# Performance work log

Measured on AMD Instinct MI355X. Metric: run time of the kernel, lower is better.

Reference implementation:

```python
import jax, jax.numpy as jnp
import numpy as np

T = 8192
C = 768
HEAD = 64

def setup_inputs() -> dict:
    key = jax.random.key(0)
    k0, k1, k2, k3 = jax.random.split(key, 4)
    tokens = jax.random.normal(k0, (T, C), dtype=jnp.float32)
    Wk = jax.random.normal(k1, (C, HEAD), dtype=jnp.float32) * (1.0 / np.sqrt(C))
    Wq = jax.random.normal(k2, (C, HEAD), dtype=jnp.float32) * (1.0 / np.sqrt(C))
    Wv = jax.random.normal(k3, (C, HEAD), dtype=jnp.float32) * (1.0 / np.sqrt(C))
    return {"tokens": tokens, "Wk": Wk, "Wq": Wq, "Wv": Wv}

def reference(tokens, Wk, Wq, Wv):
    # Single-head causal attention, faithful to source (scale = C**0.5, a multiply).
    keys = tokens @ Wk          # [T, H]
    queries = tokens @ Wq       # [T, H]
    values = tokens @ Wv        # [T, H]
    c = tokens.shape[-1]
    wei = (queries @ keys.T) * (c ** 0.5)                 # [T, T]
    causal = jnp.tril(jnp.ones((tokens.shape[0], tokens.shape[0]), dtype=bool))
    wei = jnp.where(causal, wei, -jnp.inf)
    wei = jax.nn.softmax(wei, axis=-1)
    return wei @ values         # [T, H]; dropout inactive (training=False)
```

## Files before the change

### kernel.cpp

```cpp
#include <hip/hip_runtime.h>
#include <math.h>

#define T_TOK 8192
#define C_DIM 768
#define H_DIM 64
#define SCALE_LOG2E (27.712812921102035f * 1.4426950408889634f)
#define NSPLIT 4

typedef _Float16 half8 __attribute__((ext_vector_type(8)));
typedef float floatx4 __attribute__((ext_vector_type(4)));

#define MFMA16(a, b, c) __builtin_amdgcn_mfma_f32_16x16x32_f16(a, b, c, 0, 0, 0)
#define WAIT_LGKM0() __builtin_amdgcn_s_waitcnt(0xC07F)
#define EXP2F(x) __builtin_amdgcn_exp2f(x)

typedef __attribute__((address_space(3))) void lds_void;
typedef const __attribute__((address_space(1))) void gbl_void;
#define GLOAD16(gp, lp) \
    __builtin_amdgcn_global_load_lds((gbl_void*)(gp), (lds_void*)(lp), 16, 0, 0)

template <int K> struct IC { static constexpr int v = K; };


__global__ __launch_bounds__(64) void wconvert_kernel(
    const float* __restrict__ Wk, const float* __restrict__ Wq,
    const float* __restrict__ Wv, _Float16* __restrict__ WF)
{
    const int b = blockIdx.x;
    const int mat = b / 96, rem = b % 96, kt = rem >> 2, nb = rem & 3;
    const int lane = threadIdx.x & 63, l15 = lane & 15, quad = lane >> 4;
    const float* __restrict__ W = (mat == 0) ? Wk : (mat == 1) ? Wq : Wv;

    half8 h, l;
#pragma unroll
    for (int j = 0; j < 8; ++j) {
        const float v = W[(kt * 32 + quad * 8 + j) * H_DIM + nb * 16 + l15];
        const _Float16 hv = (_Float16)v;
        h[j] = hv;
        l[j] = (_Float16)(v - (float)hv);
    }
    _Float16* dst = WF + ((((size_t)mat * 24 + kt) * 4 + nb) * 2) * 512 + lane * 8;
    *(half8*)dst = h;
    *(half8*)(dst + 512) = l;
}

__global__ __launch_bounds__(64, 1) void proj_kernel(
    const float* __restrict__ tokens, const _Float16* __restrict__ WF,
    _Float16* __restrict__ KF, _Float16* __restrict__ QF,
    _Float16* __restrict__ VF)
{
    __shared__ __align__(16) char smemraw[40960];
    const int b = blockIdx.x;
    const int lane = threadIdx.x & 63, l15 = lane & 15, quad = lane >> 4;
    const int row0 = b * 32;

    floatx4 acc[3][2][4];
#pragma unroll
    for (int mat = 0; mat < 3; ++mat)
#pragma unroll
        for (int mb = 0; mb < 2; ++mb)
#pragma unroll
            for (int nb = 0; nb < 4; ++nb) acc[mat][mb][nb] = 0;

    const float* __restrict__ xb0 = tokens + (size_t)(row0 + l15) * C_DIM + quad * 8;
    const float* __restrict__ xb1 = tokens + (size_t)(row0 + 16 + l15) * C_DIM + quad * 8;


    {
        _Float16* wb0 = (_Float16*)smemraw;
#pragma unroll
        for (int nb = 0; nb < 4; ++nb) {
            const _Float16* gK = WF + (size_t)((0 * 4 + nb) * 2) * 512 + lane * 8;
            const _Float16* gQ =
                WF + (size_t)(((1 * 24) * 4 + nb) * 2) * 512 + lane * 8;
            const _Float16* gV =
                WF + (size_t)(((2 * 24) * 4 + nb) * 2) * 512 + lane * 8;
            GLOAD16(gK,       wb0 + (nb * 2 + 0) * 512);
            GLOAD16(gK + 512, wb0 + (nb * 2 + 1) * 512);
            GLOAD16(gQ,       wb0 + (8 + nb * 2 + 0) * 512);
            GLOAD16(gQ + 512, wb0 + (8 + nb * 2 + 1) * 512);
            GLOAD16(gV,       wb0 + (16 + nb) * 512);
        }
    }
    __builtin_amdgcn_sched_barrier(0);
    float4 tf[4][4];
#pragma unroll
    for (int d = 0; d < 4; ++d) {
        tf[d][0] = *(const float4*)(xb0 + d * 32);
        tf[d][1] = *(const float4*)(xb0 + d * 32 + 4);
        tf[d][2] = *(const float4*)(xb1 + d * 32);
        tf[d][3] = *(const float4*)(xb1 + d * 32 + 4);
    }
    __builtin_amdgcn_sched_barrier(0);

    auto iter = [&](auto kc) {
        constexpr int kt = decltype(kc)::v;
        constexpr int slot = kt & 3;
        constexpr int curb = kt & 1;
        _Float16* wb  = (_Float16*)(smemraw + curb * 20480);
        _Float16* wbn = (_Float16*)(smemraw + (curb ^ 1) * 20480);

        __builtin_amdgcn_sched_barrier(0);
        const float4 x0 = tf[slot][0], x1 = tf[slot][1];
        const float4 x2 = tf[slot][2], x3 = tf[slot][3];
        __builtin_amdgcn_sched_barrier(0);

        if constexpr (kt < 23) {
            constexpr int ktn = kt + 1;
#pragma unroll
            for (int nb = 0; nb < 4; ++nb) {
                const _Float16* gK =
                    WF + (size_t)((ktn * 4 + nb) * 2) * 512 + lane * 8;
                const _Float16* gQ =
                    WF + (size_t)(((24 + ktn) * 4 + nb) * 2) * 512 + lane * 8;
                const _Float16* gV =
                    WF + (size_t)(((48 + ktn) * 4 + nb) * 2) * 512 + lane * 8;
                GLOAD16(gK,       wbn + (nb * 2 + 0) * 512);
                GLOAD16(gK + 512, wbn + (nb * 2 + 1) * 512);
                GLOAD16(gQ,       wbn + (8 + nb * 2 + 0) * 512);
                GLOAD16(gQ + 512, wbn + (8 + nb * 2 + 1) * 512);
                GLOAD16(gV,       wbn + (16 + nb) * 512);
            }
        }
        __builtin_amdgcn_sched_barrier(0);
        if constexpr (kt + 4 < 24) {
            constexpr int ktf = kt + 4;
            tf[slot][0] = *(const float4*)(xb0 + ktf * 32);
            tf[slot][1] = *(const float4*)(xb0 + ktf * 32 + 4);
            tf[slot][2] = *(const float4*)(xb1 + ktf * 32);
            tf[slot][3] = *(const float4*)(xb1 + ktf * 32 + 4);
        }
        __builtin_amdgcn_sched_barrier(0);
        constexpr int VMN = (kt == 0)
            ? 40
            : ((kt <= 20 ? 4 : 0) + (kt <= 22 ? 20 : 0) + (kt <= 19 ? 4 : 0));
        asm volatile("s_waitcnt vmcnt(%0)" ::"n"(VMN));
        __builtin_amdgcn_sched_barrier(0);

        half8 ah[2], al[2];
        {
            const float xs0[8] = {x0.x, x0.y, x0.z, x0.w, x1.x, x1.y, x1.z, x1.w};
            const float xs1[8] = {x2.x, x2.y, x2.z, x2.w, x3.x, x3.y, x3.z, x3.w};
#pragma unroll
            for (int e = 0; e < 8; ++e) {
                _Float16 hv = (_Float16)xs0[e];
                ah[0][e] = hv;
                al[0][e] = (_Float16)(xs0[e] - (float)hv);
                hv = (_Float16)xs1[e];
                ah[1][e] = hv;
                al[1][e] = (_Float16)(xs1[e] - (float)hv);
            }
        }
        const _Float16* wp = wb + lane * 8;
#pragma unroll
        for (int nb = 0; nb < 4; ++nb) {
            const half8 kh = *(const half8*)(wp + (nb * 2 + 0) * 512);
            const half8 kl = *(const half8*)(wp + (nb * 2 + 1) * 512);
            const half8 qh = *(const half8*)(wp + (8 + nb * 2 + 0) * 512);
            const half8 ql = *(const half8*)(wp + (8 + nb * 2 + 1) * 512);
            const half8 vh = *(const half8*)(wp + (16 + nb) * 512);
#pragma unroll
            for (int mb = 0; mb < 2; ++mb) {
                acc[0][mb][nb] = MFMA16(ah[mb], kh, acc[0][mb][nb]);
                acc[0][mb][nb] = MFMA16(ah[mb], kl, acc[0][mb][nb]);
                acc[0][mb][nb] = MFMA16(al[mb], kh, acc[0][mb][nb]);
                acc[1][mb][nb] = MFMA16(ah[mb], qh, acc[1][mb][nb]);
                acc[1][mb][nb] = MFMA16(ah[mb], ql, acc[1][mb][nb]);
                acc[1][mb][nb] = MFMA16(al[mb], qh, acc[1][mb][nb]);
                acc[2][mb][nb] = MFMA16(ah[mb], vh, acc[2][mb][nb]);
            }
        }
    };
#define PITER(k) iter(IC<k>{});
    PITER(0)  PITER(1)  PITER(2)  PITER(3)  PITER(4)  PITER(5)
    PITER(6)  PITER(7)  PITER(8)  PITER(9)  PITER(10) PITER(11)
    PITER(12) PITER(13) PITER(14) PITER(15) PITER(16) PITER(17)
    PITER(18) PITER(19) PITER(20) PITER(21) PITER(22) PITER(23)
#undef PITER

    __builtin_amdgcn_wave_barrier();
    WAIT_LGKM0();
    __builtin_amdgcn_wave_barrier();

    float* Cb = (float*)smemraw;
#pragma unroll
    for (int mat = 0; mat < 3; ++mat)
#pragma unroll
        for (int mb = 0; mb < 2; ++mb)
#pragma unroll
            for (int nb = 0; nb < 4; ++nb)
#pragma unroll
                for (int r = 0; r < 4; ++r)
                    Cb[mat * 2176 + (mb * 16 + quad * 4 + r) * 68 + nb * 16 + l15] =
                        acc[mat][mb][nb][r];
    __builtin_amdgcn_wave_barrier();
    WAIT_LGKM0();
    __builtin_amdgcn_wave_barrier();

#pragma unroll
    for (int nbL = 0; nbL < 2; ++nbL) {
#pragma unroll
        for (int ks = 0; ks < 2; ++ks) {
            {
                const float* cp = Cb + (nbL * 16 + l15) * 68 + ks * 32 + quad * 8;
                const float4 c0 = *(const float4*)cp;
                const float4 c1 = *(const float4*)(cp + 4);
                const float cs[8] = {c0.x, c0.y, c0.z, c0.w, c1.x, c1.y, c1.z, c1.w};
                half8 h, l;
#pragma unroll
                for (int e = 0; e < 8; ++e) {
                    const _Float16 hv = (_Float16)cs[e];
                    h[e] = hv;
                    l[e] = (_Float16)(cs[e] - (float)hv);
                }
                const int t = b >> 1, nb = (b & 1) * 2 + nbL;
                _Float16* dst =
                    KF + (((size_t)(t * 4 + nb) * 2 + ks) * 2) * 512 + lane * 8;
                *(half8*)dst = h;
                *(half8*)(dst + 512) = l;
            }
            {
                const float* cp =
                    Cb + 2176 + (nbL * 16 + l15) * 68 + ks * 32 + quad * 8;
                const float4 c0 = *(const float4*)cp;
                const float4 c1 = *(const float4*)(cp + 4);
                const float cs[8] = {c0.x, c0.y, c0.z, c0.w, c1.x, c1.y, c1.z, c1.w};
                half8 h, l;
#pragma unroll
                for (int e = 0; e < 8; ++e) {
                    const _Float16 hv = (_Float16)cs[e];
                    h[e] = hv;
                    l[e] = (_Float16)(cs[e] - (float)hv);
                }
                const int rb = b * 2 + nbL;
                _Float16* dst = QF + (((size_t)rb * 2 + ks) * 2) * 512 + lane * 8;
                *(half8*)dst = h;
                *(half8*)(dst + 512) = l;
            }
        }
    }

    {
        const int t = b >> 1, ks = b & 1;
#pragma unroll
        for (int nb = 0; nb < 4; ++nb) {
            half8 h;
#pragma unroll
            for (int j = 0; j < 8; ++j)
                h[j] = (_Float16)Cb[2 * 2176 + (quad * 8 + j) * 68 + nb * 16 + l15];
            *(half8*)(VF + ((size_t)(t * 4 + nb) * 2 + ks) * 512 + lane * 8) = h;
        }
    }
}

__global__ __launch_bounds__(512, 2) void attn_mfma_kernel(
    const _Float16* __restrict__ QF, const _Float16* __restrict__ KF,
    const _Float16* __restrict__ VF,
    float* __restrict__ pm, float* __restrict__ pl, float* __restrict__ po)
{
    __shared__ __align__(16) float smemf[9216];
    _Float16* Ps = (_Float16*)smemf;

    const int w = threadIdx.x >> 6, lane = threadIdx.x & 63;
    const int l15 = lane & 15, quad = lane >> 4;
    const int mhalf = w & 1, ss = w >> 1;

    const int b = blockIdx.x;
    const int j = b & 255, hb = b >> 8;
    const int qt = (hb == 0) ? (j >> 1) : (127 - (j >> 1));
    const int sp = (hb << 1) | (j & 1);

    const int qbase = qt * 64;
    const int wrow0 = qbase + mhalf * 32;

    half8 qh[2][2], ql[2][2];
#pragma unroll
    for (int mb = 0; mb < 2; ++mb)
#pragma unroll
        for (int ks = 0; ks < 2; ++ks) {
            const int rb = qt * 4 + mhalf * 2 + mb;
            const _Float16* qp = QF + (((size_t)rb * 2 + ks) * 2) * 512 + lane * 8;
            qh[mb][ks] = *(const half8*)qp;
            ql[mb][ks] = *(const half8*)(qp + 512);
        }

    floatx4 O[2][4];
#pragma unroll
    for (int mb = 0; mb < 2; ++mb)
#pragma unroll
        for (int nb = 0; nb < 4; ++nb) O[mb][nb] = 0;
    float mreg[2][4], lreg[2][4];
#pragma unroll
    for (int mb = 0; mb < 2; ++mb)
#pragma unroll
        for (int r = 0; r < 4; ++r) { mreg[mb][r] = -INFINITY; lreg[mb][r] = 0.f; }

    const int t0 = sp + 4 * ss;
    half8 bh[4][2], bl[4][2];
    if (t0 <= qt) {
#pragma unroll
        for (int nb = 0; nb < 4; ++nb)
#pragma unroll
            for (int ks = 0; ks < 2; ++ks) {
                const _Float16* kp =
                    KF + (((size_t)(t0 * 4 + nb) * 2 + ks) * 2) * 512 + lane * 8;
                bh[nb][ks] = *(const half8*)kp;
                bl[nb][ks] = *(const half8*)(kp + 512);
            }
    }

    for (int t = t0; t <= qt; t += 16) {
        const int kb = t * 64;

        half8 v0r[4], v1r[4];
#pragma unroll
        for (int nb = 0; nb < 4; ++nb) {
            const _Float16* vp = VF + ((size_t)(t * 4 + nb) * 2) * 512 + lane * 8;
            v0r[nb] = *(const half8*)vp;
            v1r[nb] = *(const half8*)(vp + 512);
        }

        float sv[2][4][4];
#pragma unroll
        for (int mb = 0; mb < 2; ++mb)
#pragma unroll
            for (int nb = 0; nb < 4; ++nb) {
                floatx4 s = 0;
#pragma unroll
                for (int ks = 0; ks < 2; ++ks) {
                    s = MFMA16(qh[mb][ks], bh[nb][ks], s);
                    s = MFMA16(qh[mb][ks], bl[nb][ks], s);
                    s = MFMA16(ql[mb][ks], bh[nb][ks], s);
                }
#pragma unroll
                for (int r = 0; r < 4; ++r) sv[mb][nb][r] = s[r] * SCALE_LOG2E;
            }

        if (t + 16 <= qt) {
            const int tn = t + 16;
#pragma unroll
            for (int nb = 0; nb < 4; ++nb)
#pragma unroll
                for (int ks = 0; ks < 2; ++ks) {
                    const _Float16* kp =
                        KF + (((size_t)(tn * 4 + nb) * 2 + ks) * 2) * 512 + lane * 8;
                    bh[nb][ks] = *(const half8*)kp;
                    bl[nb][ks] = *(const half8*)(kp + 512);
                }
        }

        if (kb + 63 > wrow0) {
#pragma unroll
            for (int mb = 0; mb < 2; ++mb) {
                const int rowbase = wrow0 + mb * 16 + quad * 4;
#pragma unroll
                for (int nb = 0; nb < 4; ++nb) {
                    const int col = kb + nb * 16 + l15;
#pragma unroll
                    for (int r = 0; r < 4; ++r)
                        if (col > rowbase + r) sv[mb][nb][r] = -INFINITY;
                }
            }
        }

#pragma unroll
        for (int mb = 0; mb < 2; ++mb) {
#pragma unroll
            for (int r = 0; r < 4; ++r) {
                float rm = fmaxf(fmaxf(sv[mb][0][r], sv[mb][1][r]),
                                 fmaxf(sv[mb][2][r], sv[mb][3][r]));
                rm = fmaxf(rm, __shfl_xor(rm, 1));
                rm = fmaxf(rm, __shfl_xor(rm, 2));
                rm = fmaxf(rm, __shfl_xor(rm, 4));
                rm = fmaxf(rm, __shfl_xor(rm, 8));
                const float mnew = fmaxf(mreg[mb][r], rm);
                const float alpha = EXP2F(mreg[mb][r] - mnew);
                float psum = 0.f;
#pragma unroll
                for (int nb = 0; nb < 4; ++nb) {
                    const float p = EXP2F(sv[mb][nb][r] - mnew);
                    psum += p;
                    Ps[(w * 2 + mb) * 1152 + (quad * 4 + r) * 72 + nb * 16 + l15] =
                        (_Float16)p;
                }
                lreg[mb][r] = lreg[mb][r] * alpha + psum;
                mreg[mb][r] = mnew;
#pragma unroll
                for (int nb = 0; nb < 4; ++nb) O[mb][nb][r] *= alpha;
            }
        }

        __builtin_amdgcn_wave_barrier();
        WAIT_LGKM0();
        __builtin_amdgcn_wave_barrier();
        half8 pa0[2], pa1[2];
#pragma unroll
        for (int mb = 0; mb < 2; ++mb) {
            const _Float16* pp = Ps + (w * 2 + mb) * 1152 + l15 * 72 + quad * 8;
            pa0[mb] = *(const half8*)pp;
            pa1[mb] = *(const half8*)(pp + 32);
        }

#pragma unroll
        for (int nb = 0; nb < 4; ++nb) {
#pragma unroll
            for (int mb = 0; mb < 2; ++mb) {
                O[mb][nb] = MFMA16(pa0[mb], v0r[nb], O[mb][nb]);
                O[mb][nb] = MFMA16(pa1[mb], v1r[nb], O[mb][nb]);
            }
        }
        __builtin_amdgcn_wave_barrier();
    }

#pragma unroll
    for (int mb = 0; mb < 2; ++mb)
#pragma unroll
        for (int r = 0; r < 4; ++r) {
            float s = lreg[mb][r];
            s += __shfl_xor(s, 1);
            s += __shfl_xor(s, 2);
            s += __shfl_xor(s, 4);
            s += __shfl_xor(s, 8);
            lreg[mb][r] = s;
        }

    __syncthreads();
    if (ss >= 2) {
        const int slot = ss - 2;
#pragma unroll
        for (int mb = 0; mb < 2; ++mb)
#pragma unroll
            for (int r = 0; r < 4; ++r) {
                const int row32 = mb * 16 + quad * 4 + r;
                const int sidx = (slot * 2 + mhalf) * 32 + row32;
#pragma unroll
                for (int nb = 0; nb < 4; ++nb)
                    smemf[sidx * 64 + nb * 16 + l15] = O[mb][nb][r];
                if (l15 == 0) {
                    smemf[8192 + sidx] = mreg[mb][r];
                    smemf[8320 + sidx] = lreg[mb][r];
                }
            }
    }
    __syncthreads();
    if (ss < 2) {
        const int slot = ss;
#pragma unroll
        for (int mb = 0; mb < 2; ++mb)
#pragma unroll
            for (int r = 0; r < 4; ++r) {
                const int row32 = mb * 16 + quad * 4 + r;
                const int sidx = (slot * 2 + mhalf) * 32 + row32;
                const float m1 = mreg[mb][r], l1 = lreg[mb][r];
                const float m2 = smemf[8192 + sidx];
                const float l2 = smemf[8320 + sidx];
                const float mm = fmaxf(m1, m2);
                const float a1 = (m1 == -INFINITY) ? 0.f : EXP2F(m1 - mm);
                const float a2 = (m2 == -INFINITY) ? 0.f : EXP2F(m2 - mm);
#pragma unroll
                for (int nb = 0; nb < 4; ++nb)
                    O[mb][nb][r] = O[mb][nb][r] * a1 +
                                   smemf[sidx * 64 + nb * 16 + l15] * a2;
                mreg[mb][r] = mm;
                lreg[mb][r] = l1 * a1 + l2 * a2;
            }
    }
    __syncthreads();
    if (ss == 1) {
#pragma unroll
        for (int mb = 0; mb < 2; ++mb)
#pragma unroll
            for (int r = 0; r < 4; ++r) {
                const int row32 = mb * 16 + quad * 4 + r;
                const int sidx = mhalf * 32 + row32;
#pragma unroll
                for (int nb = 0; nb < 4; ++nb)
                    smemf[sidx * 64 + nb * 16 + l15] = O[mb][nb][r];
                if (l15 == 0) {
                    smemf[8192 + sidx] = mreg[mb][r];
                    smemf[8320 + sidx] = lreg[mb][r];
                }
            }
    }
    __syncthreads();
    if (ss == 0) {
        const int pidx = qt * NSPLIT + sp;
#pragma unroll
        for (int mb = 0; mb < 2; ++mb)
#pragma unroll
            for (int r = 0; r < 4; ++r) {
                const int row32 = mb * 16 + quad * 4 + r;
                const int sidx = mhalf * 32 + row32;
                const float m1 = mreg[mb][r], l1 = lreg[mb][r];
                const float m2 = smemf[8192 + sidx];
                const float l2 = smemf[8320 + sidx];
                const float mm = fmaxf(m1, m2);
                const float a1 = (m1 == -INFINITY) ? 0.f : EXP2F(m1 - mm);
                const float a2 = (m2 == -INFINITY) ? 0.f : EXP2F(m2 - mm);
                const int row = mhalf * 32 + row32;
                float* dst = po + ((size_t)pidx * 64 + row) * 64;
#pragma unroll
                for (int nb = 0; nb < 4; ++nb)
                    dst[nb * 16 + l15] =
                        O[mb][nb][r] * a1 + smemf[sidx * 64 + nb * 16 + l15] * a2;
                if (l15 == 0) {
                    pm[pidx * 64 + row] = mm;
                    pl[pidx * 64 + row] = l1 * a1 + l2 * a2;
                }
            }
    }
}

__global__ __launch_bounds__(256) void combine_kernel(
    const float* __restrict__ pm, const float* __restrict__ pl,
    const float* __restrict__ po, float* __restrict__ out)
{
    const int vid = blockIdx.x * 256 + threadIdx.x;
    const int row = vid >> 4;
    const int d4  = vid & 15;
    const int qt  = row >> 6;
    const int r   = row & 63;

    float mm = -INFINITY;
#pragma unroll
    for (int s = 0; s < NSPLIT; ++s)
        mm = fmaxf(mm, pm[(qt * NSPLIT + s) * 64 + r]);
    float L = 0.f;
    float4 val = make_float4(0.f, 0.f, 0.f, 0.f);
#pragma unroll
    for (int s = 0; s < NSPLIT; ++s) {
        const int p = (qt * NSPLIT + s) * 64 + r;
        const float mp = pm[p];
        const float sc = (mp > -INFINITY) ? EXP2F(mp - mm) : 0.f;
        L += pl[p] * sc;
        const float4 v = *(const float4*)(po + (size_t)p * H_DIM + d4 * 4);
        val.x += v.x * sc; val.y += v.y * sc;
        val.z += v.z * sc; val.w += v.w * sc;
    }
    const float inv = 1.0f / L;
    float4 o; o.x = val.x * inv; o.y = val.y * inv;
    o.z = val.z * inv; o.w = val.w * inv;
    *(float4*)(out + (size_t)row * H_DIM + d4 * 4) = o;
}

extern "C" void kernel_launch(void* const* d_in, const int* in_sizes, int n_in,
                              void* d_out, int out_size, void* d_ws, size_t ws_size,
                              hipStream_t stream)
{
    const float* tokens = (const float*)d_in[0];
    const float* Wk = (const float*)d_in[1];
    const float* Wq = (const float*)d_in[2];
    const float* Wv = (const float*)d_in[3];
    float* out = (float*)d_out;

    char* ws = (char*)d_ws;
    const size_t MB = 1024 * 1024;
    _Float16* WF = (_Float16*)(ws + 0 * MB);
    _Float16* KF = (_Float16*)(ws + 1 * MB);
    _Float16* QF = (_Float16*)(ws + 3 * MB);
    _Float16* VF = (_Float16*)(ws + 5 * MB);
    float* pm = (float*)(ws + 6 * MB);
    float* pl = (float*)(ws + 6 * MB + 128 * 1024);
    float* po = (float*)(ws + 6 * MB + 256 * 1024);

    wconvert_kernel<<<288, 64, 0, stream>>>(Wk, Wq, Wv, WF);

    proj_kernel<<<256, 64, 0, stream>>>(tokens, WF, KF, QF, VF);

    attn_mfma_kernel<<<128 * NSPLIT, 512, 0, stream>>>(QF, KF, VF, pm, pl, po);

    combine_kernel<<<T_TOK * H_DIM / 4 / 256, 256, 0, stream>>>(pm, pl, po, out);
}
```

Measured before the change: 136.1 us.

## Split projection K-dimension across two waves with LDS reduction

The projection kernel moves from one wave to two waves per block. Each wave handles half of the 768-wide reduction, 12 k-tiles each, with its own double-buffered LDS weight region. The partial accumulators are then summed through LDS after __syncthreads, and each wave writes half of the outputs. This shortens the serial MFMA chain per block and doubles parallelism on 256 blocks, at the cost of twice the LDS use and an extra reduction pass.

```diff
diff --git a/kernel.cpp b/kernel.cpp
--- a/kernel.cpp
+++ b/kernel.cpp
@@ -44,15 +44,18 @@
     *(half8*)(dst + 512) = l;
 }
 
-__global__ __launch_bounds__(64, 1) void proj_kernel(
+__global__ __launch_bounds__(128, 1) void proj_kernel(
     const float* __restrict__ tokens, const _Float16* __restrict__ WF,
     _Float16* __restrict__ KF, _Float16* __restrict__ QF,
     _Float16* __restrict__ VF)
 {
-    __shared__ __align__(16) char smemraw[40960];
+    __shared__ __align__(16) char smemraw[81920];
     const int b = blockIdx.x;
-    const int lane = threadIdx.x & 63, l15 = lane & 15, quad = lane >> 4;
+    const int tid = threadIdx.x;
+    const int w = tid >> 6;
+    const int lane = tid & 63, l15 = lane & 15, quad = lane >> 4;
     const int row0 = b * 32;
+    const int kt0 = w * 12;
 
     floatx4 acc[3][2][4];
 #pragma unroll
@@ -62,24 +65,28 @@
 #pragma unroll
             for (int nb = 0; nb < 4; ++nb) acc[mat][mb][nb] = 0;
 
-    const float* __restrict__ xb0 = tokens + (size_t)(row0 + l15) * C_DIM + quad * 8;
-    const float* __restrict__ xb1 = tokens + (size_t)(row0 + 16 + l15) * C_DIM + quad * 8;
+    const float* __restrict__ xb0 =
+        tokens + (size_t)(row0 + l15) * C_DIM + kt0 * 32 + quad * 8;
+    const float* __restrict__ xb1 =
+        tokens + (size_t)(row0 + 16 + l15) * C_DIM + kt0 * 32 + quad * 8;
+
+    _Float16* const wavebuf = (_Float16*)(smemraw + w * 40960);
 
 
     {
-        _Float16* wb0 = (_Float16*)smemraw;
 #pragma unroll
         for (int nb = 0; nb < 4; ++nb) {
-            const _Float16* gK = WF + (size_t)((0 * 4 + nb) * 2) * 512 + lane * 8;
+            const _Float16* gK =
+                WF + (size_t)((kt0 * 4 + nb) * 2) * 512 + lane * 8;
             const _Float16* gQ =
-                WF + (size_t)(((1 * 24) * 4 + nb) * 2) * 512 + lane * 8;
+                WF + (size_t)(((24 + kt0) * 4 + nb) * 2) * 512 + lane * 8;
             const _Float16* gV =
-                WF + (size_t)(((2 * 24) * 4 + nb) * 2) * 512 + lane * 8;
-            GLOAD16(gK,       wb0 + (nb * 2 + 0) * 512);
-            GLOAD16(gK + 512, wb0 + (nb * 2 + 1) * 512);
-            GLOAD16(gQ,       wb0 + (8 + nb * 2 + 0) * 512);
-            GLOAD16(gQ + 512, wb0 + (8 + nb * 2 + 1) * 512);
-            GLOAD16(gV,       wb0 + (16 + nb) * 512);
+                WF + (size_t)(((48 + kt0) * 4 + nb) * 2) * 512 + lane * 8;
+            GLOAD16(gK,       wavebuf + (nb * 2 + 0) * 512);
+            GLOAD16(gK + 512, wavebuf + (nb * 2 + 1) * 512);
+            GLOAD16(gQ,       wavebuf + (8 + nb * 2 + 0) * 512);
+            GLOAD16(gQ + 512, wavebuf + (8 + nb * 2 + 1) * 512);
+            GLOAD16(gV,       wavebuf + (16 + nb) * 512);
         }
     }
     __builtin_amdgcn_sched_barrier(0);
@@ -94,19 +101,19 @@
     __builtin_amdgcn_sched_barrier(0);
 
     auto iter = [&](auto kc) {
-        constexpr int kt = decltype(kc)::v;
-        constexpr int slot = kt & 3;
-        constexpr int curb = kt & 1;
-        _Float16* wb  = (_Float16*)(smemraw + curb * 20480);
-        _Float16* wbn = (_Float16*)(smemraw + (curb ^ 1) * 20480);
+        constexpr int ktl = decltype(kc)::v;
+        constexpr int slot = ktl & 3;
+        constexpr int curb = ktl & 1;
+        _Float16* wb  = wavebuf + curb * 10240;
+        _Float16* wbn = wavebuf + (curb ^ 1) * 10240;
 
         __builtin_amdgcn_sched_barrier(0);
         const float4 x0 = tf[slot][0], x1 = tf[slot][1];
         const float4 x2 = tf[slot][2], x3 = tf[slot][3];
         __builtin_amdgcn_sched_barrier(0);
 
-        if constexpr (kt < 23) {
-            constexpr int ktn = kt + 1;
+        if constexpr (ktl < 11) {
+            const int ktn = kt0 + ktl + 1;
 #pragma unroll
             for (int nb = 0; nb < 4; ++nb) {
                 const _Float16* gK =
@@ -123,17 +130,17 @@
             }
         }
         __builtin_amdgcn_sched_barrier(0);
-        if constexpr (kt + 4 < 24) {
-            constexpr int ktf = kt + 4;
+        if constexpr (ktl + 4 < 12) {
+            constexpr int ktf = ktl + 4;
             tf[slot][0] = *(const float4*)(xb0 + ktf * 32);
             tf[slot][1] = *(const float4*)(xb0 + ktf * 32 + 4);
             tf[slot][2] = *(const float4*)(xb1 + ktf * 32);
             tf[slot][3] = *(const float4*)(xb1 + ktf * 32 + 4);
         }
         __builtin_amdgcn_sched_barrier(0);
-        constexpr int VMN = (kt == 0)
+        constexpr int VMN = (ktl == 0)
             ? 40
-            : ((kt <= 20 ? 4 : 0) + (kt <= 22 ? 20 : 0) + (kt <= 19 ? 4 : 0));
+            : ((ktl <= 8 ? 4 : 0) + (ktl <= 10 ? 20 : 0) + (ktl <= 7 ? 4 : 0));
         asm volatile("s_waitcnt vmcnt(%0)" ::"n"(VMN));
         __builtin_amdgcn_sched_barrier(0);
 
@@ -174,15 +181,13 @@
 #define PITER(k) iter(IC<k>{});
     PITER(0)  PITER(1)  PITER(2)  PITER(3)  PITER(4)  PITER(5)
     PITER(6)  PITER(7)  PITER(8)  PITER(9)  PITER(10) PITER(11)
-    PITER(12) PITER(13) PITER(14) PITER(15) PITER(16) PITER(17)
-    PITER(18) PITER(19) PITER(20) PITER(21) PITER(22) PITER(23)
 #undef PITER
 
-    __builtin_amdgcn_wave_barrier();
-    WAIT_LGKM0();
-    __builtin_amdgcn_wave_barrier();
-
-    float* Cb = (float*)smemraw;
+    __syncthreads();
+
+    float* Cb0 = (float*)smemraw;
+    float* Cb1 = (float*)(smemraw + 26112);
+    float* Cbw = w ? Cb1 : Cb0;
 #pragma unroll
     for (int mat = 0; mat < 3; ++mat)
 #pragma unroll
@@ -191,21 +196,23 @@
             for (int nb = 0; nb < 4; ++nb)
 #pragma unroll
                 for (int r = 0; r < 4; ++r)
-                    Cb[mat * 2176 + (mb * 16 + quad * 4 + r) * 68 + nb * 16 + l15] =
+                    Cbw[mat * 2176 + (mb * 16 + quad * 4 + r) * 68 + nb * 16 + l15] =
                         acc[mat][mb][nb][r];
-    __builtin_amdgcn_wave_barrier();
-    WAIT_LGKM0();
-    __builtin_amdgcn_wave_barrier();
-
-#pragma unroll
-    for (int nbL = 0; nbL < 2; ++nbL) {
+    __syncthreads();
+
+    {
+        const int nbL = w;
 #pragma unroll
         for (int ks = 0; ks < 2; ++ks) {
             {
-                const float* cp = Cb + (nbL * 16 + l15) * 68 + ks * 32 + quad * 8;
-                const float4 c0 = *(const float4*)cp;
-                const float4 c1 = *(const float4*)(cp + 4);
-                const float cs[8] = {c0.x, c0.y, c0.z, c0.w, c1.x, c1.y, c1.z, c1.w};
+                const int off = (nbL * 16 + l15) * 68 + ks * 32 + quad * 8;
+                const float4 a0 = *(const float4*)(Cb0 + off);
+                const float4 a1 = *(const float4*)(Cb0 + off + 4);
+                const float4 b0 = *(const float4*)(Cb1 + off);
+                const float4 b1 = *(const float4*)(Cb1 + off + 4);
+                const float cs[8] = {a0.x + b0.x, a0.y + b0.y, a0.z + b0.z,
+                                     a0.w + b0.w, a1.x + b1.x, a1.y + b1.y,
+                                     a1.z + b1.z, a1.w + b1.w};
                 half8 h, l;
 #pragma unroll
                 for (int e = 0; e < 8; ++e) {
@@ -220,11 +227,15 @@
                 *(half8*)(dst + 512) = l;
             }
             {
-                const float* cp =
-                    Cb + 2176 + (nbL * 16 + l15) * 68 + ks * 32 + quad * 8;
-                const float4 c0 = *(const float4*)cp;
-                const float4 c1 = *(const float4*)(cp + 4);
-                const float cs[8] = {c0.x, c0.y, c0.z, c0.w, c1.x, c1.y, c1.z, c1.w};
+                const int off =
+                    2176 + (nbL * 16 + l15) * 68 + ks * 32 + quad * 8;
+                const float4 a0 = *(const float4*)(Cb0 + off);
+                const float4 a1 = *(const float4*)(Cb0 + off + 4);
+                const float4 b0 = *(const float4*)(Cb1 + off);
+                const float4 b1 = *(const float4*)(Cb1 + off + 4);
+                const float cs[8] = {a0.x + b0.x, a0.y + b0.y, a0.z + b0.z,
+                                     a0.w + b0.w, a1.x + b1.x, a1.y + b1.y,
+                                     a1.z + b1.z, a1.w + b1.w};
                 half8 h, l;
 #pragma unroll
                 for (int e = 0; e < 8; ++e) {
@@ -243,11 +254,14 @@
     {
         const int t = b >> 1, ks = b & 1;
 #pragma unroll
-        for (int nb = 0; nb < 4; ++nb) {
+        for (int nbi = 0; nbi < 2; ++nbi) {
+            const int nb = w * 2 + nbi;
             half8 h;
 #pragma unroll
-            for (int j = 0; j < 8; ++j)
-                h[j] = (_Float16)Cb[2 * 2176 + (quad * 8 + j) * 68 + nb * 16 + l15];
+            for (int j = 0; j < 8; ++j) {
+                const int off = 2 * 2176 + (quad * 8 + j) * 68 + nb * 16 + l15;
+                h[j] = (_Float16)(Cb0[off] + Cb1[off]);
+            }
             *(half8*)(VF + ((size_t)(t * 4 + nb) * 2 + ks) * 512 + lane * 8) = h;
         }
     }
@@ -565,7 +579,7 @@
 
     wconvert_kernel<<<288, 64, 0, stream>>>(Wk, Wq, Wv, WF);
 
-    proj_kernel<<<256, 64, 0, stream>>>(tokens, WF, KF, QF, VF);
+    proj_kernel<<<256, 128, 0, stream>>>(tokens, WF, KF, QF, VF);
 
     attn_mfma_kernel<<<128 * NSPLIT, 512, 0, stream>>>(QF, KF, VF, pm, pl, po);
 
```

Measured after the change: 125.8 us. 7.5% less time.
